# Kernel optimization log

Hardware: AMD Instinct MI355X
Metric: run time of the kernel (lower is better)

Reference implementation:

```python
import jax, jax.numpy as jnp
import numpy as np

B, T, E, H, V = 64, 32, 512, 512, 16000


def setup_inputs() -> dict:
    key = jax.random.key(0)
    ks = jax.random.split(key, 9)
    s_e = 1.0 / np.sqrt(E)
    s_h = 1.0 / np.sqrt(H)
    return {
        "features": jax.random.normal(ks[0], (B, E), dtype=jnp.float32),
        "captions": jax.random.randint(ks[1], (B, T), 0, V, dtype=jnp.int64),
        "emb": jax.random.normal(ks[2], (V, E), dtype=jnp.float32) * 0.02,
        "W_ih": jax.random.normal(ks[3], (4 * H, E), dtype=jnp.float32) * s_e,
        "W_hh": jax.random.normal(ks[4], (4 * H, H), dtype=jnp.float32) * s_h,
        "b_ih": jax.random.normal(ks[5], (4 * H,), dtype=jnp.float32) * s_h,
        "b_hh": jax.random.normal(ks[6], (4 * H,), dtype=jnp.float32) * s_h,
        "W_lin": jax.random.normal(ks[7], (V, H), dtype=jnp.float32) * s_h,
        "b_lin": jax.random.normal(ks[8], (V,), dtype=jnp.float32) * s_h,
    }


def reference(features, captions, emb, W_ih, W_hh, b_ih, b_hh, W_lin, b_lin):
    # features: [B, E]; captions: [B, T] int. Faithful to original: input at
    # t=0 is features, at t>=1 it is embedding(captions[:, t]) (not t-1).
    Bn, Tn = captions.shape
    Hn = W_hh.shape[1]
    emb_cap = emb[captions]                                   # [B, T, E]
    x_seq = jnp.concatenate([features[:, None, :], emb_cap[:, 1:, :]], axis=1)
    # Precompute input projection for all timesteps: [B, T, 4H]
    x_proj = jnp.einsum("bte,ge->btg", x_seq, W_ih) + b_ih + b_hh

    def step(carry, xp_t):                                    # xp_t: [B, 4H]
        h, c = carry
        gates = xp_t + h @ W_hh.T
        i, f, g, o = jnp.split(gates, 4, axis=-1)             # PyTorch ifgo order
        i = jax.nn.sigmoid(i)
        f = jax.nn.sigmoid(f)
        g = jnp.tanh(g)
        o = jax.nn.sigmoid(o)
        c = f * c + i * g
        h = o * jnp.tanh(c)
        return (h, c), h

    h0 = jnp.zeros((Bn, Hn), dtype=features.dtype)
    c0 = jnp.zeros((Bn, Hn), dtype=features.dtype)
    _, hs = jax.lax.scan(step, (h0, c0), jnp.swapaxes(x_proj, 0, 1))  # hs: [T, B, H]
    hs = jnp.swapaxes(hs, 0, 1)                               # [B, T, H]
    logits = jnp.einsum("bth,vh->btv", hs, W_lin) + b_lin     # [B, T, V]
    return logits
```

## Files before the change

### kernel.cpp

```cpp
#include <hip/hip_runtime.h>
#include <hip/hip_bf16.h>


typedef __attribute__((ext_vector_type(8))) short short8v;
typedef __attribute__((ext_vector_type(4))) short short4v;
typedef __attribute__((ext_vector_type(4))) float float4v;
typedef __attribute__((ext_vector_type(4))) int   int4v;

static __device__ __forceinline__ short f2bf(float v) {
    __hip_bfloat16 b = __float2bfloat16(v);
    return *reinterpret_cast<short*>(&b);
}
static __device__ __forceinline__ float bf2f(short s) {
    __hip_bfloat16 b = *reinterpret_cast<__hip_bfloat16*>(&s);
    return __bfloat162float(b);
}


__global__ __launch_bounds__(256) void prep_x_kernel(
    const float* __restrict__ features, const int* __restrict__ captions,
    const float* __restrict__ emb, short* __restrict__ A1)
{
    int m = blockIdx.x;
    int b = m >> 5, t = m & 31;
    const float* src = (t == 0) ? (features + (long)b * 512)
                                : (emb + (long)captions[b * 32 + t] * 512);
    long base = (long)m * 1536;
    for (int k = threadIdx.x; k < 512; k += 256) {
        float v = src[k];
        short hi = f2bf(v);
        short lo = f2bf(v - bf2f(hi));
        A1[base + k]        = hi;
        A1[base + 512 + k]  = lo;
        A1[base + 1024 + k] = hi;
    }
}

__global__ __launch_bounds__(256) void prep_w_kernel(
    const float* __restrict__ W_ih, short* __restrict__ B1)
{
    int n = blockIdx.x;
    long base = (long)n * 1536;
    const float* src = W_ih + (long)n * 512;
    for (int k = threadIdx.x; k < 512; k += 256) {
        float v = src[k];
        short hi = f2bf(v);
        short lo = f2bf(v - bf2f(hi));
        B1[base + k]        = hi;
        B1[base + 512 + k]  = hi;
        B1[base + 1024 + k] = lo;
    }
}

__global__ __launch_bounds__(256) void prep_bias_kernel(
    const float* __restrict__ b_ih, const float* __restrict__ b_hh,
    float* __restrict__ biasc, int* __restrict__ flags)
{
    int g = blockIdx.x * 256 + threadIdx.x;
    if (g < 2048) biasc[g] = b_ih[g] + b_hh[g];
    if (g < 512)  flags[g] = 0;
}

__global__ __launch_bounds__(256) void prep_wlin_kernel(
    const float* __restrict__ W_lin, short* __restrict__ Wl)
{
    int v = blockIdx.x;
    long base = (long)v * 512;
    for (int k = threadIdx.x; k < 512; k += 256) {
        Wl[base + k] = f2bf(W_lin[base + k]);
    }
}

#define AF2_FRAGS 8192
#define W3_FRAGS_PER_BLK 4096

static __device__ __forceinline__ int frag2_idx(int tile, int k, int row15, int isLo)
{
    return ((tile * 32 + (k >> 5) + isLo * 16) * 64
            + ((k >> 2) & 3) * 16 + row15) * 8
           + (k & 3) + ((k >> 4) & 1) * 4;
}

__global__ __launch_bounds__(256) void prep_whh_kernel(
    const float* __restrict__ W_hh, short* __restrict__ W2)
{
    int n  = blockIdx.x;
    int s  = n >> 9, jg = n & 511;
    int ob = jg >> 3, u = jg & 7;
    int nl = s * 8 + u;
    int nt = nl >> 4, rr = nl & 15;
    short* dst = W2 + (long)ob * (W3_FRAGS_PER_BLK * 8);
    for (int k0 = threadIdx.x; k0 < 512; k0 += 256) {
        float v  = W_hh[(long)n * 512 + k0];
        short hi = f2bf(v);
        short lo = f2bf(v - bf2f(hi));
        dst[frag2_idx(nt, k0, rr, 0)] = hi;
        dst[frag2_idx(nt, k0, rr, 1)] = lo;
    }
}

#define GBK 64
#define GPAD 8
#define GLDT (GBK + GPAD)

__global__ __launch_bounds__(256) void gemm_bf16_kernel(
    const short* __restrict__ A, const short* __restrict__ B,
    const float* __restrict__ bias, float* __restrict__ C,
    int M, int N, int K)
{
    __shared__ short As[128 * GLDT];
    __shared__ short Bs[128 * GLDT];

    const int tid  = threadIdx.x;
    const int bm   = blockIdx.x, bn = blockIdx.y;
    const int lane = tid & 63, wave = tid >> 6;
    const int wm   = wave >> 1, wn = wave & 1;
    const int r    = lane & 15, q = lane >> 4;

    float4v acc[4][4];
#pragma unroll
    for (int i = 0; i < 4; ++i)
#pragma unroll
        for (int j = 0; j < 4; ++j) acc[i][j] = (float4v)(0.0f);

    const long arow0 = (long)bm * 128;
    const long brow0 = (long)bn * 128;

    for (int kt = 0; kt < K; kt += GBK) {
        __syncthreads();
#pragma unroll
        for (int it = 0; it < 4; ++it) {
            int task = tid + it * 256;
            int row = task >> 3, seg = task & 7;
            const short* gA = A + (arow0 + row) * (long)K + kt + seg * 8;
            *(short8v*)&As[row * GLDT + seg * 8] = *(const short8v*)gA;
            const short* gB = B + (brow0 + row) * (long)K + kt + seg * 8;
            *(short8v*)&Bs[row * GLDT + seg * 8] = *(const short8v*)gB;
        }
        __syncthreads();
#pragma unroll
        for (int kc = 0; kc < GBK; kc += 32) {
            short8v af[4], bf[4];
#pragma unroll
            for (int i = 0; i < 4; ++i) {
                int arow = wm * 64 + i * 16 + r;
                union { short4v h[2]; short8v v; } ua;
                ua.h[0] = *(short4v*)&As[arow * GLDT + kc + q * 4];
                ua.h[1] = *(short4v*)&As[arow * GLDT + kc + 16 + q * 4];
                af[i] = ua.v;
                int brow = wn * 64 + i * 16 + r;
                union { short4v h[2]; short8v v; } ub;
                ub.h[0] = *(short4v*)&Bs[brow * GLDT + kc + q * 4];
                ub.h[1] = *(short4v*)&Bs[brow * GLDT + kc + 16 + q * 4];
                bf[i] = ub.v;
            }
#pragma unroll
            for (int i = 0; i < 4; ++i)
#pragma unroll
                for (int j = 0; j < 4; ++j)
                    acc[i][j] = __builtin_amdgcn_mfma_f32_16x16x32_bf16(
                        af[i], bf[j], acc[i][j], 0, 0, 0);
        }
    }

#pragma unroll
    for (int j = 0; j < 4; ++j) {
        int col = bn * 128 + wn * 64 + j * 16 + r;
        float bv = bias[col];
#pragma unroll
        for (int i = 0; i < 4; ++i) {
            int row0 = bm * 128 + wm * 64 + i * 16 + q * 4;
#pragma unroll
            for (int reg = 0; reg < 4; ++reg) {
                C[(long)(row0 + reg) * N + col] = acc[i][j][reg] + bv;
            }
        }
    }
}

__global__ __launch_bounds__(512, 1) void fused_lstm_logits_kernel(
    const float* __restrict__ x_proj, const short* __restrict__ W2,
    short* __restrict__ Af, short* __restrict__ hs2,
    int* __restrict__ flags, const short* __restrict__ Wl,
    const float* __restrict__ b_lin, float* __restrict__ out)
{
    __shared__ __align__(16) short Wf[W3_FRAGS_PER_BLK * 8];
    __shared__ float gl[32 * 65];
    __shared__ short Hs[64][12];
    __shared__ short Ls[64][12];
    __shared__ short As[128 * GLDT];
    __shared__ short Bs[128 * GLDT];

    const int tid  = threadIdx.x;
    const int bid  = blockIdx.x;
    const int lane = tid & 63;
    const int wave = tid >> 6;
    const int r    = lane & 15, q = lane >> 4;
    const int frep = (bid & 7) * 64;

    if (bid < 64) {
        const int mt   = wave & 3;
        const int nt   = wave >> 2;
        const int j0   = bid * 8;
        const int aq   = bid & 3;
        const int kt0  = bid >> 2;

        {
            const short8v* src = (const short8v*)W2 + (size_t)bid * W3_FRAGS_PER_BLK;
            short8v* dst = (short8v*)Wf;
            for (int i = tid; i < W3_FRAGS_PER_BLK; i += 512) dst[i] = src[i];
        }
        __syncthreads();

        const int bb  = lane;
        const int ub  = wave;
        const int jj  = j0 + ub;
        float c_reg = 0.0f;

        const int rdt  = (tid >> 7) & 1;
        const int rmt  = (tid >> 5) & 3;
        const int rrb  = (tid >> 1) & 15;
        const int rhf  = tid & 1;
        const int rbb  = rmt * 16 + rrb;
        const int rq5  = (2 * aq + rhf) & 3;
        const size_t rfrag =
            (size_t)((rmt * 32 + kt0 + rdt * 16) * 64 + rq5 * 16 + rrb);
        const size_t roff = rfrag * 8 + (size_t)(aq >> 1) * 4;

        const short8v* Bw = (const short8v*)Wf + nt * 32 * 64 + lane;

        float xc0, xc1, xc2, xc3;
        {
            const float* xp = x_proj + ((size_t)bb * 32 + 0) * 2048 + jj;
            xc0 = xp[0]; xc1 = xp[512]; xc2 = xp[1024]; xc3 = xp[1536];
        }

        for (int t = 0; t < 32; ++t) {
            float xn0 = 0.f, xn1 = 0.f, xn2 = 0.f, xn3 = 0.f;
            if (t < 31) {
                const float* xp = x_proj + ((size_t)bb * 32 + (t + 1)) * 2048 + jj;
                xn0 = xp[0]; xn1 = xp[512]; xn2 = xp[1024]; xn3 = xp[1536];
            }

            float4v acc = (float4v)(0.0f);
            if (t > 0) {
                const short8v* Ab = (const short8v*)Af
                    + (size_t)(t - 1) * AF2_FRAGS + mt * 32 * 64 + lane;
                short8v Ahi[16], Alo[16];

                unsigned long long ready;
                {
                    int myf = __hip_atomic_load(&flags[frep + lane], __ATOMIC_RELAXED,
                                                __HIP_MEMORY_SCOPE_AGENT);
                    ready = __ballot(myf >= t);
                }
#pragma unroll
                for (int g = 0; g < 4; ++g) {
                    const unsigned long long need = 0xFFFFull << (g * 16);
                    while ((ready & need) != need) {
                        int myf = __hip_atomic_load(&flags[frep + lane], __ATOMIC_RELAXED,
                                                    __HIP_MEMORY_SCOPE_AGENT);
                        ready = __ballot(myf >= t);
                    }
                    asm volatile("" ::: "memory");
#pragma unroll
                    for (int k = 0; k < 4; ++k) {
                        Ahi[g * 4 + k] = Ab[(g * 4 + k) * 64];
                        Alo[g * 4 + k] = Ab[(16 + g * 4 + k) * 64];
                    }
                }

                float4v a0 = (float4v)(0.0f), a1 = (float4v)(0.0f), a2 = (float4v)(0.0f);
#pragma unroll
                for (int kt = 0; kt < 16; ++kt) {
                    short8v Bhi = Bw[kt * 64];
                    short8v Blo = Bw[(16 + kt) * 64];
                    a0 = __builtin_amdgcn_mfma_f32_16x16x32_bf16(Ahi[kt], Bhi, a0, 0, 0, 0);
                    a1 = __builtin_amdgcn_mfma_f32_16x16x32_bf16(Alo[kt], Bhi, a1, 0, 0, 0);
                    a2 = __builtin_amdgcn_mfma_f32_16x16x32_bf16(Ahi[kt], Blo, a2, 0, 0, 0);
                }
                acc = a0 + a1 + a2;
            }

            __syncthreads();
#pragma unroll
            for (int reg = 0; reg < 4; ++reg)
                gl[(nt * 16 + r) * 65 + mt * 16 + q * 4 + reg] = acc[reg];
            __syncthreads();

            float iv = gl[(0  + ub) * 65 + bb] + xc0;
            float fv = gl[(8  + ub) * 65 + bb] + xc1;
            float gv = gl[(16 + ub) * 65 + bb] + xc2;
            float ov = gl[(24 + ub) * 65 + bb] + xc3;
            float ig = 1.f / (1.f + __expf(-iv));
            float fg = 1.f / (1.f + __expf(-fv));
            float gg = tanhf(gv);
            float og = 1.f / (1.f + __expf(-ov));
            float cn = fg * c_reg + ig * gg;
            float hn = og * tanhf(cn);
            c_reg = cn;

            short hi = f2bf(hn);
            Hs[bb][ub] = hi;
            if (t < 31) Ls[bb][ub] = f2bf(hn - bf2f(hi));
            __syncthreads();

            if (tid < 256) {
                if (t < 31) {
                    const short* src = rdt ? &Ls[rbb][rhf * 4] : &Hs[rbb][rhf * 4];
                    short s0 = src[0], s1 = src[1], s2 = src[2], s3 = src[3];
                    unsigned lo32 = (unsigned short)s0 | ((unsigned)(unsigned short)s1 << 16);
                    unsigned hi32 = (unsigned short)s2 | ((unsigned)(unsigned short)s3 << 16);
                    long long pv = ((long long)hi32 << 32) | (long long)lo32;
                    short* dst = Af + (size_t)t * (AF2_FRAGS * 8) + roff;
                    asm volatile("global_store_dwordx2 %0, %1, off sc0 sc1"
                                 :: "v"(dst), "v"(pv) : "memory");
                }
                if (tid < 64) {
                    const short* hp = &Hs[tid][0];
                    int4v pv;
                    pv.x = (int)((unsigned short)hp[0] | ((unsigned)(unsigned short)hp[1] << 16));
                    pv.y = (int)((unsigned short)hp[2] | ((unsigned)(unsigned short)hp[3] << 16));
                    pv.z = (int)((unsigned short)hp[4] | ((unsigned)(unsigned short)hp[5] << 16));
                    pv.w = (int)((unsigned short)hp[6] | ((unsigned)(unsigned short)hp[7] << 16));
                    char* dst2 = (char*)(hs2 + ((size_t)t * 64 + tid) * 512 + j0);
                    asm volatile("global_store_dwordx4 %0, %1, off sc0 sc1"
                                 :: "v"(dst2), "v"(pv) : "memory");
                }
                asm volatile("s_waitcnt vmcnt(0)" ::: "memory");
            }
            __syncthreads();
            if (tid == 0) {
#pragma unroll
                for (int rp = 0; rp < 8; ++rp)
                    __hip_atomic_store(&flags[rp * 64 + bid], t + 1,
                                       __ATOMIC_RELAXED, __HIP_MEMORY_SCOPE_AGENT);
            }

            xc0 = xn0; xc1 = xn1; xc2 = xn2; xc3 = xn3;
        }
    } else {
        const int w   = bid - 64;
        const int wm2 = wave >> 2;
        const int wn2 = wave & 3;

        for (int task = w; task < 2000; task += 192) {
            const int bm = task / 125;
            const int bn = task % 125;
            const int target = 2 * bm + 2;

            if (tid < 64) {
                while (true) {
                    int f = __hip_atomic_load(&flags[frep + tid], __ATOMIC_RELAXED,
                                              __HIP_MEMORY_SCOPE_AGENT);
                    if (!__any(f < target)) break;
                    __builtin_amdgcn_s_sleep(16);
                }
            }
            __syncthreads();

            float4v acc[4][2];
#pragma unroll
            for (int i = 0; i < 4; ++i)
#pragma unroll
                for (int j = 0; j < 2; ++j) acc[i][j] = (float4v)(0.0f);

            const long arow0 = (long)bm * 128;
            const long brow0 = (long)bn * 128;

            for (int kt = 0; kt < 512; kt += GBK) {
                __syncthreads();
#pragma unroll
                for (int it = 0; it < 2; ++it) {
                    int task2 = tid + it * 512;
                    int row = task2 >> 3, seg = task2 & 7;
                    const short* gA = hs2 + (arow0 + row) * 512L + kt + seg * 8;
                    *(short8v*)&As[row * GLDT + seg * 8] = *(const short8v*)gA;
                    const short* gB = Wl + (brow0 + row) * 512L + kt + seg * 8;
                    *(short8v*)&Bs[row * GLDT + seg * 8] = *(const short8v*)gB;
                }
                __syncthreads();
#pragma unroll
                for (int kc = 0; kc < GBK; kc += 32) {
                    short8v af[4], bf[2];
#pragma unroll
                    for (int i = 0; i < 4; ++i) {
                        int arow = wm2 * 64 + i * 16 + r;
                        union { short4v h[2]; short8v v; } ua;
                        ua.h[0] = *(short4v*)&As[arow * GLDT + kc + q * 4];
                        ua.h[1] = *(short4v*)&As[arow * GLDT + kc + 16 + q * 4];
                        af[i] = ua.v;
                    }
#pragma unroll
                    for (int j = 0; j < 2; ++j) {
                        int brow = wn2 * 32 + j * 16 + r;
                        union { short4v h[2]; short8v v; } ub;
                        ub.h[0] = *(short4v*)&Bs[brow * GLDT + kc + q * 4];
                        ub.h[1] = *(short4v*)&Bs[brow * GLDT + kc + 16 + q * 4];
                        bf[j] = ub.v;
                    }
#pragma unroll
                    for (int i = 0; i < 4; ++i)
#pragma unroll
                        for (int j = 0; j < 2; ++j)
                            acc[i][j] = __builtin_amdgcn_mfma_f32_16x16x32_bf16(
                                af[i], bf[j], acc[i][j], 0, 0, 0);
                }
            }

#pragma unroll
            for (int j = 0; j < 2; ++j) {
                int col = bn * 128 + wn2 * 32 + j * 16 + r;
                float bv = b_lin[col];
#pragma unroll
                for (int i = 0; i < 4; ++i) {
                    int lr0 = wm2 * 64 + i * 16 + q * 4;
#pragma unroll
                    for (int reg = 0; reg < 4; ++reg) {
                        int m  = bm * 128 + lr0 + reg;
                        int tt = m >> 6, bb2 = m & 63;
                        out[((long)bb2 * 32 + tt) * 16000 + col] = acc[i][j][reg] + bv;
                    }
                }
            }
            __syncthreads();
        }
    }
}

extern "C" void kernel_launch(void* const* d_in, const int* in_sizes, int n_in,
                              void* d_out, int out_size, void* d_ws, size_t ws_size,
                              hipStream_t stream) {
    const float* features = (const float*)d_in[0];
    const int*   captions = (const int*)d_in[1];
    const float* emb      = (const float*)d_in[2];
    const float* W_ih     = (const float*)d_in[3];
    const float* W_hh     = (const float*)d_in[4];
    const float* b_ih     = (const float*)d_in[5];
    const float* b_hh     = (const float*)d_in[6];
    const float* W_lin    = (const float*)d_in[7];
    const float* b_lin    = (const float*)d_in[8];
    float* out = (float*)d_out;

    char* ws = (char*)d_ws;
    float* x_proj = (float*)ws;  ws += 2048L * 2048 * 4;
    short* A1     = (short*)ws;  ws += 2048L * 1536 * 2;
    short* B1     = (short*)ws;  ws += 2048L * 1536 * 2;
    short* Wl     = (short*)ws;  ws += 16000L * 512 * 2;
    short* hs2    = (short*)ws;  ws += 2048L * 512 * 2;
    float* biasc  = (float*)ws;  ws += 2048 * 4;
    int*   flags  = (int*)ws;    ws += 2048;
    short* Af2    = (short*)ws;  ws += 31L * AF2_FRAGS * 8 * 2;

    prep_x_kernel<<<2048, 256, 0, stream>>>(features, captions, emb, A1);
    prep_w_kernel<<<2048, 256, 0, stream>>>(W_ih, B1);
    prep_bias_kernel<<<8, 256, 0, stream>>>(b_ih, b_hh, biasc, flags);
    prep_wlin_kernel<<<16000, 256, 0, stream>>>(W_lin, Wl);

    dim3 gA(16, 16);
    gemm_bf16_kernel<<<gA, 256, 0, stream>>>(A1, B1, biasc, x_proj,
                                             2048, 2048, 1536);

    prep_whh_kernel<<<2048, 256, 0, stream>>>(W_hh, B1);

    fused_lstm_logits_kernel<<<256, 512, 0, stream>>>(
        x_proj, B1, Af2, hs2, flags, Wl, b_lin, out);
}
```

Before: 253.8 us.

## Publish recurrent step flags early and validate hidden-state fragments via poison sentinel

The LSTM blocks now set the per-step readiness flag right after issuing the hidden-state fragment stores, without waiting for those stores to complete behind a block barrier. Consumers check that the fragments they loaded hold no 0xFFFF sentinel, which a new prep kernel writes over the whole buffer, and reload until every fragment is valid. A second flag array, set after the full barrier, keeps ordering for the logits GEMM workers that read hs2. This cuts latency on the serial recurrence critical path, at the cost of an extra poison kernel, a data-dependent reload loop, and a sentinel check that could misfire if a real bf16 pair ever equals the all-ones pattern (a NaN encoding).

```diff
diff --git a/kernel.cpp b/kernel.cpp
--- a/kernel.cpp
+++ b/kernel.cpp
@@ -58,7 +58,7 @@
 {
     int g = blockIdx.x * 256 + threadIdx.x;
     if (g < 2048) biasc[g] = b_ih[g] + b_hh[g];
-    if (g < 512)  flags[g] = 0;
+    if (g < 1024) flags[g] = 0;
 }
 
 __global__ __launch_bounds__(256) void prep_wlin_kernel(
@@ -99,6 +99,18 @@
     }
 }
 
+__global__ __launch_bounds__(256) void poison_af_kernel(short* __restrict__ Af)
+{
+    int idx = blockIdx.x * 256 + threadIdx.x;
+    const int total = 31 * AF2_FRAGS * 8 * 2 / 16;
+    if (idx < total) {
+        int4v pv = {-1, -1, -1, -1};
+        char* p = (char*)Af + (size_t)idx * 16;
+        asm volatile("global_store_dwordx4 %0, %1, off sc0 sc1"
+                     :: "v"(p), "v"(pv) : "memory");
+    }
+}
+
 #define GBK 64
 #define GPAD 8
 #define GLDT (GBK + GPAD)
@@ -246,7 +258,8 @@
             if (t > 0) {
                 const short8v* Ab = (const short8v*)Af
                     + (size_t)(t - 1) * AF2_FRAGS + mt * 32 * 64 + lane;
-                short8v Ahi[16], Alo[16];
+                union frag_u { int4v i; short8v s; };
+                frag_u fha[16], fla[16];
 
                 unsigned long long ready;
                 {
@@ -265,8 +278,34 @@
                     asm volatile("" ::: "memory");
 #pragma unroll
                     for (int k = 0; k < 4; ++k) {
-                        Ahi[g * 4 + k] = Ab[(g * 4 + k) * 64];
-                        Alo[g * 4 + k] = Ab[(16 + g * 4 + k) * 64];
+                        fha[g * 4 + k].s = Ab[(g * 4 + k) * 64];
+                        fla[g * 4 + k].s = Ab[(16 + g * 4 + k) * 64];
+                    }
+                }
+
+                {
+                    const char* abase = (const char*)Ab;
+                    while (true) {
+                        int ok = 1;
+#pragma unroll
+                        for (int k = 0; k < 16; ++k) {
+                            ok &= (fha[k].i.x != -1) & (fha[k].i.z != -1)
+                                & (fla[k].i.x != -1) & (fla[k].i.z != -1);
+                        }
+                        if (__all(ok)) break;
+#pragma unroll
+                        for (int k = 0; k < 16; ++k) {
+                            asm volatile("global_load_dwordx4 %0, %1, off sc0 sc1"
+                                         : "=v"(fha[k].i)
+                                         : "v"(abase + (size_t)k * 1024)
+                                         : "memory");
+                            asm volatile("global_load_dwordx4 %0, %1, off sc0 sc1"
+                                         : "=v"(fla[k].i)
+                                         : "v"(abase + 16384 + (size_t)k * 1024)
+                                         : "memory");
+                        }
+                        asm volatile("s_waitcnt vmcnt(0)" ::: "memory");
+                        __builtin_amdgcn_sched_barrier(0);
                     }
                 }
 
@@ -275,9 +314,9 @@
                 for (int kt = 0; kt < 16; ++kt) {
                     short8v Bhi = Bw[kt * 64];
                     short8v Blo = Bw[(16 + kt) * 64];
-                    a0 = __builtin_amdgcn_mfma_f32_16x16x32_bf16(Ahi[kt], Bhi, a0, 0, 0, 0);
-                    a1 = __builtin_amdgcn_mfma_f32_16x16x32_bf16(Alo[kt], Bhi, a1, 0, 0, 0);
-                    a2 = __builtin_amdgcn_mfma_f32_16x16x32_bf16(Ahi[kt], Blo, a2, 0, 0, 0);
+                    a0 = __builtin_amdgcn_mfma_f32_16x16x32_bf16(fha[kt].s, Bhi, a0, 0, 0, 0);
+                    a1 = __builtin_amdgcn_mfma_f32_16x16x32_bf16(fla[kt].s, Bhi, a1, 0, 0, 0);
+                    a2 = __builtin_amdgcn_mfma_f32_16x16x32_bf16(fha[kt].s, Blo, a2, 0, 0, 0);
                 }
                 acc = a0 + a1 + a2;
             }
@@ -305,35 +344,41 @@
             if (t < 31) Ls[bb][ub] = f2bf(hn - bf2f(hi));
             __syncthreads();
 
-            if (tid < 256) {
-                if (t < 31) {
-                    const short* src = rdt ? &Ls[rbb][rhf * 4] : &Hs[rbb][rhf * 4];
-                    short s0 = src[0], s1 = src[1], s2 = src[2], s3 = src[3];
-                    unsigned lo32 = (unsigned short)s0 | ((unsigned)(unsigned short)s1 << 16);
-                    unsigned hi32 = (unsigned short)s2 | ((unsigned)(unsigned short)s3 << 16);
-                    long long pv = ((long long)hi32 << 32) | (long long)lo32;
-                    short* dst = Af + (size_t)t * (AF2_FRAGS * 8) + roff;
-                    asm volatile("global_store_dwordx2 %0, %1, off sc0 sc1"
-                                 :: "v"(dst), "v"(pv) : "memory");
-                }
-                if (tid < 64) {
-                    const short* hp = &Hs[tid][0];
-                    int4v pv;
-                    pv.x = (int)((unsigned short)hp[0] | ((unsigned)(unsigned short)hp[1] << 16));
-                    pv.y = (int)((unsigned short)hp[2] | ((unsigned)(unsigned short)hp[3] << 16));
-                    pv.z = (int)((unsigned short)hp[4] | ((unsigned)(unsigned short)hp[5] << 16));
-                    pv.w = (int)((unsigned short)hp[6] | ((unsigned)(unsigned short)hp[7] << 16));
-                    char* dst2 = (char*)(hs2 + ((size_t)t * 64 + tid) * 512 + j0);
-                    asm volatile("global_store_dwordx4 %0, %1, off sc0 sc1"
-                                 :: "v"(dst2), "v"(pv) : "memory");
-                }
-                asm volatile("s_waitcnt vmcnt(0)" ::: "memory");
-            }
-            __syncthreads();
-            if (tid == 0) {
+            if (t < 31 && tid < 256) {
+                const short* src = rdt ? &Ls[rbb][rhf * 4] : &Hs[rbb][rhf * 4];
+                short s0 = src[0], s1 = src[1], s2 = src[2], s3 = src[3];
+                unsigned lo32 = (unsigned short)s0 | ((unsigned)(unsigned short)s1 << 16);
+                unsigned hi32 = (unsigned short)s2 | ((unsigned)(unsigned short)s3 << 16);
+                long long pv = ((long long)hi32 << 32) | (long long)lo32;
+                short* dst = Af + (size_t)t * (AF2_FRAGS * 8) + roff;
+                asm volatile("global_store_dwordx2 %0, %1, off sc0 sc1"
+                             :: "v"(dst), "v"(pv) : "memory");
+            }
+            if (t < 31 && tid == 0) {
 #pragma unroll
                 for (int rp = 0; rp < 8; ++rp)
                     __hip_atomic_store(&flags[rp * 64 + bid], t + 1,
+                                       __ATOMIC_RELAXED, __HIP_MEMORY_SCOPE_AGENT);
+            }
+            if (tid < 64) {
+                const short* hp = &Hs[tid][0];
+                int4v pv;
+                pv.x = (int)((unsigned short)hp[0] | ((unsigned)(unsigned short)hp[1] << 16));
+                pv.y = (int)((unsigned short)hp[2] | ((unsigned)(unsigned short)hp[3] << 16));
+                pv.z = (int)((unsigned short)hp[4] | ((unsigned)(unsigned short)hp[5] << 16));
+                pv.w = (int)((unsigned short)hp[6] | ((unsigned)(unsigned short)hp[7] << 16));
+                char* dst2 = (char*)(hs2 + ((size_t)t * 64 + tid) * 512 + j0);
+                asm volatile("global_store_dwordx4 %0, %1, off sc0 sc1"
+                             :: "v"(dst2), "v"(pv) : "memory");
+            }
+            if (tid < 256)
+                asm volatile("s_waitcnt vmcnt(0)" ::: "memory");
+            __builtin_amdgcn_s_barrier();
+            asm volatile("" ::: "memory");
+            if (tid == 0) {
+#pragma unroll
+                for (int rp = 0; rp < 8; ++rp)
+                    __hip_atomic_store(&flags[512 + rp * 64 + bid], t + 1,
                                        __ATOMIC_RELAXED, __HIP_MEMORY_SCOPE_AGENT);
             }
 
@@ -351,7 +396,7 @@
 
             if (tid < 64) {
                 while (true) {
-                    int f = __hip_atomic_load(&flags[frep + tid], __ATOMIC_RELAXED,
+                    int f = __hip_atomic_load(&flags[512 + frep + tid], __ATOMIC_RELAXED,
                                               __HIP_MEMORY_SCOPE_AGENT);
                     if (!__any(f < target)) break;
                     __builtin_amdgcn_s_sleep(16);
@@ -449,13 +494,14 @@
     short* Wl     = (short*)ws;  ws += 16000L * 512 * 2;
     short* hs2    = (short*)ws;  ws += 2048L * 512 * 2;
     float* biasc  = (float*)ws;  ws += 2048 * 4;
-    int*   flags  = (int*)ws;    ws += 2048;
+    int*   flags  = (int*)ws;    ws += 4096;
     short* Af2    = (short*)ws;  ws += 31L * AF2_FRAGS * 8 * 2;
 
     prep_x_kernel<<<2048, 256, 0, stream>>>(features, captions, emb, A1);
     prep_w_kernel<<<2048, 256, 0, stream>>>(W_ih, B1);
     prep_bias_kernel<<<8, 256, 0, stream>>>(b_ih, b_hh, biasc, flags);
     prep_wlin_kernel<<<16000, 256, 0, stream>>>(W_lin, Wl);
+    poison_af_kernel<<<992, 256, 0, stream>>>(Af2);
 
     dim3 gA(16, 16);
     gemm_bf16_kernel<<<gA, 256, 0, stream>>>(A1, B1, biasc, x_proj,
```

Result: slower. 480.6 us (+89.4%).

## Fuse input-projection GEMM into persistent LSTM kernel with per-tile readiness counters

Applied to the files above, without the earlier changes.

The separate x_proj GEMM and the W_hh prep kernel are removed. Worker blocks of the persistent kernel now compute the input projection in time-major row tiles, publish completion through atomic counters, and then continue with the logits tiles. The LSTM blocks convert W_hh into LDS fragments themselves and wait on those counters before reading each timestep's projection. This aims to overlap the projection GEMM with the recurrence and to cut two launches, at the cost of spin-wait synchronisation and the added risk of ordering or visibility bugs.

```diff
diff --git a/kernel.cpp b/kernel.cpp
--- a/kernel.cpp
+++ b/kernel.cpp
@@ -22,7 +22,7 @@
     const float* __restrict__ emb, short* __restrict__ A1)
 {
     int m = blockIdx.x;
-    int b = m >> 5, t = m & 31;
+    int t = m >> 6, b = m & 63;
     const float* src = (t == 0) ? (features + (long)b * 512)
                                 : (emb + (long)captions[b * 32 + t] * 512);
     long base = (long)m * 1536;
@@ -58,7 +58,7 @@
 {
     int g = blockIdx.x * 256 + threadIdx.x;
     if (g < 2048) biasc[g] = b_ih[g] + b_hh[g];
-    if (g < 512)  flags[g] = 0;
+    if (g < 640)  flags[g] = 0;
 }
 
 __global__ __launch_bounds__(256) void prep_wlin_kernel(
@@ -81,105 +81,14 @@
            + (k & 3) + ((k >> 4) & 1) * 4;
 }
 
-__global__ __launch_bounds__(256) void prep_whh_kernel(
-    const float* __restrict__ W_hh, short* __restrict__ W2)
-{
-    int n  = blockIdx.x;
-    int s  = n >> 9, jg = n & 511;
-    int ob = jg >> 3, u = jg & 7;
-    int nl = s * 8 + u;
-    int nt = nl >> 4, rr = nl & 15;
-    short* dst = W2 + (long)ob * (W3_FRAGS_PER_BLK * 8);
-    for (int k0 = threadIdx.x; k0 < 512; k0 += 256) {
-        float v  = W_hh[(long)n * 512 + k0];
-        short hi = f2bf(v);
-        short lo = f2bf(v - bf2f(hi));
-        dst[frag2_idx(nt, k0, rr, 0)] = hi;
-        dst[frag2_idx(nt, k0, rr, 1)] = lo;
-    }
-}
-
 #define GBK 64
 #define GPAD 8
 #define GLDT (GBK + GPAD)
 
-__global__ __launch_bounds__(256) void gemm_bf16_kernel(
-    const short* __restrict__ A, const short* __restrict__ B,
-    const float* __restrict__ bias, float* __restrict__ C,
-    int M, int N, int K)
-{
-    __shared__ short As[128 * GLDT];
-    __shared__ short Bs[128 * GLDT];
-
-    const int tid  = threadIdx.x;
-    const int bm   = blockIdx.x, bn = blockIdx.y;
-    const int lane = tid & 63, wave = tid >> 6;
-    const int wm   = wave >> 1, wn = wave & 1;
-    const int r    = lane & 15, q = lane >> 4;
-
-    float4v acc[4][4];
-#pragma unroll
-    for (int i = 0; i < 4; ++i)
-#pragma unroll
-        for (int j = 0; j < 4; ++j) acc[i][j] = (float4v)(0.0f);
-
-    const long arow0 = (long)bm * 128;
-    const long brow0 = (long)bn * 128;
-
-    for (int kt = 0; kt < K; kt += GBK) {
-        __syncthreads();
-#pragma unroll
-        for (int it = 0; it < 4; ++it) {
-            int task = tid + it * 256;
-            int row = task >> 3, seg = task & 7;
-            const short* gA = A + (arow0 + row) * (long)K + kt + seg * 8;
-            *(short8v*)&As[row * GLDT + seg * 8] = *(const short8v*)gA;
-            const short* gB = B + (brow0 + row) * (long)K + kt + seg * 8;
-            *(short8v*)&Bs[row * GLDT + seg * 8] = *(const short8v*)gB;
-        }
-        __syncthreads();
-#pragma unroll
-        for (int kc = 0; kc < GBK; kc += 32) {
-            short8v af[4], bf[4];
-#pragma unroll
-            for (int i = 0; i < 4; ++i) {
-                int arow = wm * 64 + i * 16 + r;
-                union { short4v h[2]; short8v v; } ua;
-                ua.h[0] = *(short4v*)&As[arow * GLDT + kc + q * 4];
-                ua.h[1] = *(short4v*)&As[arow * GLDT + kc + 16 + q * 4];
-                af[i] = ua.v;
-                int brow = wn * 64 + i * 16 + r;
-                union { short4v h[2]; short8v v; } ub;
-                ub.h[0] = *(short4v*)&Bs[brow * GLDT + kc + q * 4];
-                ub.h[1] = *(short4v*)&Bs[brow * GLDT + kc + 16 + q * 4];
-                bf[i] = ub.v;
-            }
-#pragma unroll
-            for (int i = 0; i < 4; ++i)
-#pragma unroll
-                for (int j = 0; j < 4; ++j)
-                    acc[i][j] = __builtin_amdgcn_mfma_f32_16x16x32_bf16(
-                        af[i], bf[j], acc[i][j], 0, 0, 0);
-        }
-    }
-
-#pragma unroll
-    for (int j = 0; j < 4; ++j) {
-        int col = bn * 128 + wn * 64 + j * 16 + r;
-        float bv = bias[col];
-#pragma unroll
-        for (int i = 0; i < 4; ++i) {
-            int row0 = bm * 128 + wm * 64 + i * 16 + q * 4;
-#pragma unroll
-            for (int reg = 0; reg < 4; ++reg) {
-                C[(long)(row0 + reg) * N + col] = acc[i][j][reg] + bv;
-            }
-        }
-    }
-}
-
 __global__ __launch_bounds__(512, 1) void fused_lstm_logits_kernel(
-    const float* __restrict__ x_proj, const short* __restrict__ W2,
+    float* __restrict__ x_proj, const float* __restrict__ W_hh,
+    const short* __restrict__ A1, const short* __restrict__ B1,
+    const float* __restrict__ biasc,
     short* __restrict__ Af, short* __restrict__ hs2,
     int* __restrict__ flags, const short* __restrict__ Wl,
     const float* __restrict__ b_lin, float* __restrict__ out)
@@ -196,7 +105,9 @@
     const int lane = tid & 63;
     const int wave = tid >> 6;
     const int r    = lane & 15, q = lane >> 4;
-    const int frep = (bid & 7) * 64;
+    const int frep   = (bid & 7) * 64;
+    const int frep16 = (bid & 7) * 16;
+    int* __restrict__ xpc = flags + 512;
 
     if (bid < 64) {
         const int mt   = wave & 3;
@@ -205,10 +116,15 @@
         const int aq   = bid & 3;
         const int kt0  = bid >> 2;
 
-        {
-            const short8v* src = (const short8v*)W2 + (size_t)bid * W3_FRAGS_PER_BLK;
-            short8v* dst = (short8v*)Wf;
-            for (int i = tid; i < W3_FRAGS_PER_BLK; i += 512) dst[i] = src[i];
+        for (int i = 0; i < 32; ++i) {
+            int nl = i;
+            int s2 = nl >> 3, u2 = nl & 7;
+            int nt2 = nl >> 4, rr2 = nl & 15;
+            float v = W_hh[((long)s2 * 512 + j0 + u2) * 512 + tid];
+            short hi2 = f2bf(v);
+            short lo2 = f2bf(v - bf2f(hi2));
+            Wf[frag2_idx(nt2, tid, rr2, 0)] = hi2;
+            Wf[frag2_idx(nt2, tid, rr2, 1)] = lo2;
         }
         __syncthreads();
 
@@ -229,17 +145,34 @@
 
         const short8v* Bw = (const short8v*)Wf + nt * 32 * 64 + lane;
 
+        if (tid == 0) {
+            while (__hip_atomic_load(&xpc[frep16 + 0], __ATOMIC_RELAXED,
+                                     __HIP_MEMORY_SCOPE_AGENT) < 16)
+                __builtin_amdgcn_s_sleep(4);
+        }
+        __syncthreads();
+
         float xc0, xc1, xc2, xc3;
         {
-            const float* xp = x_proj + ((size_t)bb * 32 + 0) * 2048 + jj;
+            const float* xp = x_proj + ((size_t)0 * 64 + bb) * 2048 + jj;
             xc0 = xp[0]; xc1 = xp[512]; xc2 = xp[1024]; xc3 = xp[1536];
         }
+        int xpn = 16;
 
         for (int t = 0; t < 32; ++t) {
             float xn0 = 0.f, xn1 = 0.f, xn2 = 0.f, xn3 = 0.f;
             if (t < 31) {
-                const float* xp = x_proj + ((size_t)bb * 32 + (t + 1)) * 2048 + jj;
+                int nbm = (t + 1) >> 1;
+                if (xpn < 16) {
+                    while (__hip_atomic_load(&xpc[frep16 + nbm], __ATOMIC_RELAXED,
+                                             __HIP_MEMORY_SCOPE_AGENT) < 16)
+                        __builtin_amdgcn_s_sleep(2);
+                }
+                const float* xp = x_proj + ((size_t)(t + 1) * 64 + bb) * 2048 + jj;
                 xn0 = xp[0]; xn1 = xp[512]; xn2 = xp[1024]; xn3 = xp[1536];
+                int fbm = (t + 2) >> 1; if (fbm > 15) fbm = 15;
+                xpn = __hip_atomic_load(&xpc[frep16 + fbm], __ATOMIC_RELAXED,
+                                        __HIP_MEMORY_SCOPE_AGENT);
             }
 
             float4v acc = (float4v)(0.0f);
@@ -344,82 +277,163 @@
         const int wm2 = wave >> 2;
         const int wn2 = wave & 3;
 
-        for (int task = w; task < 2000; task += 192) {
-            const int bm = task / 125;
-            const int bn = task % 125;
-            const int target = 2 * bm + 2;
-
-            if (tid < 64) {
-                while (true) {
-                    int f = __hip_atomic_load(&flags[frep + tid], __ATOMIC_RELAXED,
-                                              __HIP_MEMORY_SCOPE_AGENT);
-                    if (!__any(f < target)) break;
-                    __builtin_amdgcn_s_sleep(16);
-                }
-            }
-            __syncthreads();
-
-            float4v acc[4][2];
-#pragma unroll
-            for (int i = 0; i < 4; ++i)
-#pragma unroll
-                for (int j = 0; j < 2; ++j) acc[i][j] = (float4v)(0.0f);
-
-            const long arow0 = (long)bm * 128;
-            const long brow0 = (long)bn * 128;
-
-            for (int kt = 0; kt < 512; kt += GBK) {
+        for (int task = w; task < 2256; task += 192) {
+            if (task < 256) {
+                const int bm = task >> 4;
+                const int bn = task & 15;
+
+                float4v acc[4][2];
+#pragma unroll
+                for (int i = 0; i < 4; ++i)
+#pragma unroll
+                    for (int j = 0; j < 2; ++j) acc[i][j] = (float4v)(0.0f);
+
+                const long arow0 = (long)bm * 128;
+                const long brow0 = (long)bn * 128;
+
+                for (int kt = 0; kt < 1536; kt += GBK) {
+                    __syncthreads();
+#pragma unroll
+                    for (int it = 0; it < 2; ++it) {
+                        int t2 = tid + it * 512;
+                        int row = t2 >> 3, seg = t2 & 7;
+                        const short* gA = A1 + (arow0 + row) * 1536L + kt + seg * 8;
+                        *(short8v*)&As[row * GLDT + seg * 8] = *(const short8v*)gA;
+                        const short* gB = B1 + (brow0 + row) * 1536L + kt + seg * 8;
+                        *(short8v*)&Bs[row * GLDT + seg * 8] = *(const short8v*)gB;
+                    }
+                    __syncthreads();
+#pragma unroll
+                    for (int kc = 0; kc < GBK; kc += 32) {
+                        short8v af[4], bf[2];
+#pragma unroll
+                        for (int i = 0; i < 4; ++i) {
+                            int arow = wm2 * 64 + i * 16 + r;
+                            union { short4v h[2]; short8v v; } ua;
+                            ua.h[0] = *(short4v*)&As[arow * GLDT + kc + q * 4];
+                            ua.h[1] = *(short4v*)&As[arow * GLDT + kc + 16 + q * 4];
+                            af[i] = ua.v;
+                        }
+#pragma unroll
+                        for (int j = 0; j < 2; ++j) {
+                            int brow = wn2 * 32 + j * 16 + r;
+                            union { short4v h[2]; short8v v; } ub;
+                            ub.h[0] = *(short4v*)&Bs[brow * GLDT + kc + q * 4];
+                            ub.h[1] = *(short4v*)&Bs[brow * GLDT + kc + 16 + q * 4];
+                            bf[j] = ub.v;
+                        }
+#pragma unroll
+                        for (int i = 0; i < 4; ++i)
+#pragma unroll
+                            for (int j = 0; j < 2; ++j)
+                                acc[i][j] = __builtin_amdgcn_mfma_f32_16x16x32_bf16(
+                                    af[i], bf[j], acc[i][j], 0, 0, 0);
+                    }
+                }
+
+#pragma unroll
+                for (int j = 0; j < 2; ++j) {
+                    int col = bn * 128 + wn2 * 32 + j * 16 + r;
+                    float bv = biasc[col];
+#pragma unroll
+                    for (int i = 0; i < 4; ++i) {
+                        int row0 = bm * 128 + wm2 * 64 + i * 16 + q * 4;
+#pragma unroll
+                        for (int reg = 0; reg < 4; ++reg) {
+                            float vv = acc[i][j][reg] + bv;
+                            float* dst = x_proj + (size_t)(row0 + reg) * 2048 + col;
+                            asm volatile("global_store_dword %0, %1, off sc0 sc1"
+                                         :: "v"(dst), "v"(vv) : "memory");
+                        }
+                    }
+                }
+                asm volatile("s_waitcnt vmcnt(0)" ::: "memory");
                 __syncthreads();
-#pragma unroll
-                for (int it = 0; it < 2; ++it) {
-                    int task2 = tid + it * 512;
-                    int row = task2 >> 3, seg = task2 & 7;
-                    const short* gA = hs2 + (arow0 + row) * 512L + kt + seg * 8;
-                    *(short8v*)&As[row * GLDT + seg * 8] = *(const short8v*)gA;
-                    const short* gB = Wl + (brow0 + row) * 512L + kt + seg * 8;
-                    *(short8v*)&Bs[row * GLDT + seg * 8] = *(const short8v*)gB;
+                if (tid == 0) {
+#pragma unroll
+                    for (int rp = 0; rp < 8; ++rp)
+                        __hip_atomic_fetch_add(&xpc[rp * 16 + bm], 1,
+                                               __ATOMIC_RELAXED,
+                                               __HIP_MEMORY_SCOPE_AGENT);
+                }
+            } else {
+                const int lt = task - 256;
+                const int bm = lt / 125;
+                const int bn = lt % 125;
+                const int target = 2 * bm + 2;
+
+                if (tid < 64) {
+                    while (true) {
+                        int f = __hip_atomic_load(&flags[frep + tid], __ATOMIC_RELAXED,
+                                                  __HIP_MEMORY_SCOPE_AGENT);
+                        if (!__any(f < target)) break;
+                        __builtin_amdgcn_s_sleep(16);
+                    }
                 }
                 __syncthreads();
-#pragma unroll
-                for (int kc = 0; kc < GBK; kc += 32) {
-                    short8v af[4], bf[2];
+
+                float4v acc[4][2];
+#pragma unroll
+                for (int i = 0; i < 4; ++i)
+#pragma unroll
+                    for (int j = 0; j < 2; ++j) acc[i][j] = (float4v)(0.0f);
+
+                const long arow0 = (long)bm * 128;
+                const long brow0 = (long)bn * 128;
+
+                for (int kt = 0; kt < 512; kt += GBK) {
+                    __syncthreads();
+#pragma unroll
+                    for (int it = 0; it < 2; ++it) {
+                        int t2 = tid + it * 512;
+                        int row = t2 >> 3, seg = t2 & 7;
+                        const short* gA = hs2 + (arow0 + row) * 512L + kt + seg * 8;
+                        *(short8v*)&As[row * GLDT + seg * 8] = *(const short8v*)gA;
+                        const short* gB = Wl + (brow0 + row) * 512L + kt + seg * 8;
+                        *(short8v*)&Bs[row * GLDT + seg * 8] = *(const short8v*)gB;
+                    }
+                    __syncthreads();
+#pragma unroll
+                    for (int kc = 0; kc < GBK; kc += 32) {
+                        short8v af[4], bf[2];
+#pragma unroll
+                        for (int i = 0; i < 4; ++i) {
+                            int arow = wm2 * 64 + i * 16 + r;
+                            union { short4v h[2]; short8v v; } ua;
+                            ua.h[0] = *(short4v*)&As[arow * GLDT + kc + q * 4];
+                            ua.h[1] = *(short4v*)&As[arow * GLDT + kc + 16 + q * 4];
+                            af[i] = ua.v;
+                        }
+#pragma unroll
+                        for (int j = 0; j < 2; ++j) {
+                            int brow = wn2 * 32 + j * 16 + r;
+                            union { short4v h[2]; short8v v; } ub;
+                            ub.h[0] = *(short4v*)&Bs[brow * GLDT + kc + q * 4];
+                            ub.h[1] = *(short4v*)&Bs[brow * GLDT + kc + 16 + q * 4];
+                            bf[j] = ub.v;
+                        }
+#pragma unroll
+                        for (int i = 0; i < 4; ++i)
+#pragma unroll
+                            for (int j = 0; j < 2; ++j)
+                                acc[i][j] = __builtin_amdgcn_mfma_f32_16x16x32_bf16(
+                                    af[i], bf[j], acc[i][j], 0, 0, 0);
+                    }
+                }
+
+#pragma unroll
+                for (int j = 0; j < 2; ++j) {
+                    int col = bn * 128 + wn2 * 32 + j * 16 + r;
+                    float bv = b_lin[col];
 #pragma unroll
                     for (int i = 0; i < 4; ++i) {
-                        int arow = wm2 * 64 + i * 16 + r;
-                        union { short4v h[2]; short8v v; } ua;
-                        ua.h[0] = *(short4v*)&As[arow * GLDT + kc + q * 4];
-                        ua.h[1] = *(short4v*)&As[arow * GLDT + kc + 16 + q * 4];
-                        af[i] = ua.v;
-                    }
-#pragma unroll
-                    for (int j = 0; j < 2; ++j) {
-                        int brow = wn2 * 32 + j * 16 + r;
-                        union { short4v h[2]; short8v v; } ub;
-                        ub.h[0] = *(short4v*)&Bs[brow * GLDT + kc + q * 4];
-                        ub.h[1] = *(short4v*)&Bs[brow * GLDT + kc + 16 + q * 4];
-                        bf[j] = ub.v;
-                    }
-#pragma unroll
-                    for (int i = 0; i < 4; ++i)
-#pragma unroll
-                        for (int j = 0; j < 2; ++j)
-                            acc[i][j] = __builtin_amdgcn_mfma_f32_16x16x32_bf16(
-                                af[i], bf[j], acc[i][j], 0, 0, 0);
-                }
-            }
-
-#pragma unroll
-            for (int j = 0; j < 2; ++j) {
-                int col = bn * 128 + wn2 * 32 + j * 16 + r;
-                float bv = b_lin[col];
-#pragma unroll
-                for (int i = 0; i < 4; ++i) {
-                    int lr0 = wm2 * 64 + i * 16 + q * 4;
-#pragma unroll
-                    for (int reg = 0; reg < 4; ++reg) {
-                        int m  = bm * 128 + lr0 + reg;
-                        int tt = m >> 6, bb2 = m & 63;
-                        out[((long)bb2 * 32 + tt) * 16000 + col] = acc[i][j][reg] + bv;
+                        int lr0 = wm2 * 64 + i * 16 + q * 4;
+#pragma unroll
+                        for (int reg = 0; reg < 4; ++reg) {
+                            int m  = bm * 128 + lr0 + reg;
+                            int tt = m >> 6, bb2 = m & 63;
+                            out[((long)bb2 * 32 + tt) * 16000 + col] = acc[i][j][reg] + bv;
+                        }
                     }
                 }
             }
@@ -449,7 +463,7 @@
     short* Wl     = (short*)ws;  ws += 16000L * 512 * 2;
     short* hs2    = (short*)ws;  ws += 2048L * 512 * 2;
     float* biasc  = (float*)ws;  ws += 2048 * 4;
-    int*   flags  = (int*)ws;    ws += 2048;
+    int*   flags  = (int*)ws;    ws += 4096;
     short* Af2    = (short*)ws;  ws += 31L * AF2_FRAGS * 8 * 2;
 
     prep_x_kernel<<<2048, 256, 0, stream>>>(features, captions, emb, A1);
@@ -457,12 +471,6 @@
     prep_bias_kernel<<<8, 256, 0, stream>>>(b_ih, b_hh, biasc, flags);
     prep_wlin_kernel<<<16000, 256, 0, stream>>>(W_lin, Wl);
 
-    dim3 gA(16, 16);
-    gemm_bf16_kernel<<<gA, 256, 0, stream>>>(A1, B1, biasc, x_proj,
-                                             2048, 2048, 1536);
-
-    prep_whh_kernel<<<2048, 256, 0, stream>>>(W_hh, B1);
-
     fused_lstm_logits_kernel<<<256, 512, 0, stream>>>(
-        x_proj, B1, Af2, hs2, flags, Wl, b_lin, out);
-}
+        x_proj, W_hh, A1, B1, biasc, Af2, hs2, flags, Wl, b_lin, out);
+}
```

Result: faster. 248.6 us (-2.0%).
